# Performance work log

Hardware: AMD Instinct MI355X
Metric: run time of the kernel (lower is better)

Reference implementation:

```python
import jax, jax.numpy as jnp
import numpy as np

B, N, F, H, C, NH = 4, 256, 64, 64, 32, 4
EPS = 1e-5
INF = 1e5


def setup_inputs() -> dict:
    key = jax.random.key(0)
    ks = iter(jax.random.split(key, 40))
    def rn(shape, s=0.05):
        return jax.random.normal(next(ks), shape, jnp.float32) * s
    return dict(
        h=rn((B, N, F), 1.0), x=rn((B, N, 3), 1.0), v=rn((B, N, 3), 1.0),
        # edge_model = ConcatenationFilter: Linear(2F+1->H), SiLU, Linear(H->H), SiLU
        W_e1=rn((2 * F + 1, H)), b_e1=jnp.zeros(H), W_e2=rn((H, H)), b_e2=jnp.zeros(H),
        # coefficients_mlp: Linear(H->H), SiLU, Linear(H->C)
        W_c1=rn((H, H)), b_c1=jnp.zeros(H), W_c2=rn((H, C)), b_c2=jnp.zeros(C),
        # post_norm_mlp: Linear(C->H), SiLU, Linear(H->H)
        W_p1=rn((C, H)), b_p1=jnp.zeros(H), W_p2=rn((H, H)), b_p2=jnp.zeros(H),
        # semantic_attention_mlp: Linear(H->NH), LeakyReLU(0.2)
        W_s=rn((H, NH)), b_s=jnp.zeros(NH),
        # node_mlp: Linear(NH*H + H + F -> H), SiLU, Linear(H->F)
        W_n1=rn((NH * H + H + F, H)), b_n1=jnp.zeros(H), W_n2=rn((H, F)), b_n2=jnp.zeros(F),
        # velocity_mlp: Linear(F->H), SiLU, Linear(H->1, no bias), xavier gain=0.001
        W_v1=rn((F, H)), b_v1=jnp.zeros(H), W_v2=rn((H, 1), 0.001),
        log_gamma=jnp.zeros(NH),
    )


def reference(h, x, v, W_e1, b_e1, W_e2, b_e2, W_c1, b_c1, W_c2, b_c2,
              W_p1, b_p1, W_p2, b_p2, W_s, b_s, W_n1, b_n1, W_n2, b_n2,
              W_v1, b_v1, W_v2, log_gamma):
    silu = jax.nn.silu
    f = h.shape[-1]
    n = h.shape[-2]
    # pairwise displacements: [B,i,j,3] = x_j - x_i (torch: x.unsqueeze(-3) - x.unsqueeze(-2))
    x_minus_xt = x[..., None, :, :] - x[..., :, None, :]
    nrm = jnp.sqrt(jnp.sum(x_minus_xt ** 2, -1, keepdims=True) + EPS)  # [B,i,j,1]
    # edge model: first Linear over cat([h_j, h_i, nrm]) decomposed to avoid the big concat
    lin_j = h @ W_e1[:f]           # [B,N,H]
    lin_i = h @ W_e1[f:2 * f]      # [B,N,H]
    pre = lin_j[..., None, :, :] + lin_i[..., :, None, :] + nrm * W_e1[2 * f] + b_e1
    h_e_mtx = silu(silu(pre) @ W_e2 + b_e2)  # [B,i,j,H]
    # spatial attention
    coeff = silu(h_e_mtx @ W_c1 + b_c1) @ W_c2 + b_c2          # [B,i,j,C]
    x_scaled = x_minus_xt / (nrm + EPS) ** 2                   # [B,i,j,3]
    combinations = coeff[..., None] * x_scaled[..., None, :]   # [B,i,j,C,3]
    comb_sum = combinations.sum(-3)                            # sum over j -> [B,i,C,3]
    comb_norm = jnp.sum(comb_sum ** 2, -1)                     # [B,i,C]
    h_comb = silu(comb_norm @ W_p1 + b_p1) @ W_p2 + b_p2       # [B,i,H]
    delta_v = combinations.mean(axis=(-2, -3))                 # [B,i,3]
    # velocity + coordinate update (update_coordinate=True, velocity=True)
    v = (silu(h @ W_v1 + b_v1) @ W_v2) * v
    v = delta_v + v
    x = x + v
    # combined attention over j axis (-2)
    eye = jnp.eye(n, dtype=h.dtype)[:, :, None]                # [N,N,1]
    att_e = jax.nn.softmax(-(nrm + INF * eye) * jnp.exp(log_gamma), axis=-2)  # softmin
    att_s = jax.nn.softmax(jax.nn.leaky_relu(h_e_mtx @ W_s + b_s, 0.2) - INF * eye, axis=-2)
    att = jax.nn.softmax(att_e * att_s, axis=-2)               # [B,i,j,NH]
    # head-expanded messages: (h_e_mtx[...,H,1] * att[...,1,NH]).flatten -> [B,i,j,H*NH]
    h_e_full = (h_e_mtx[..., :, None] * att[..., None, :]).reshape(h_e_mtx.shape[:-1] + (-1,))
    h_e = h_e_full.sum(-2)                                     # aggregate over j -> [B,i,H*NH]
    out = silu(jnp.concatenate([h, h_e, h_comb], -1) @ W_n1 + b_n1) @ W_n2 + b_n2
    h = h + out  # residual
    return (h, x, v)
```

## Files before the change

### kernel.cpp

```cpp
#include <hip/hip_runtime.h>

typedef unsigned short u16;
typedef unsigned int   u32;
typedef __attribute__((ext_vector_type(8))) short bf16x8;
typedef __attribute__((ext_vector_type(4))) float f32x4;

#define EPSc 1e-5f
#define INFc 1e5f

#define O_LINJ  0
#define O_LINI  262144
#define O_VSC   524288
#define O_WE2F  528384
#define O_WC1F  536576
#define O_WC2F  546816
#define O_WP1C  550912
#define O_WP2C  559104
#define O_WN2C  575488
#define O_WN1C  591872
#define O_XF    690176
#define O_VF    702464
#define O_BIAS  714752
#define O_FLAG  741536

#define B_BE2 0
#define B_BC1 64
#define B_BC2 128
#define B_BS  160
#define B_GE  164
#define B_BP1 168
#define B_BP2 232
#define B_BN1 296
#define B_BN2 360
#define B_W1L 424
#define B_BE1 488

struct P {
    const void *h, *x, *v;
    const void *We1, *be1, *We2, *be2, *Wc1, *bc1, *Wc2, *bc2;
    const void *Wp1, *bp1, *Wp2, *bp2, *Ws_, *bs_;
    const void *Wn1, *bn1, *Wn2, *bn2, *Wv1, *bv1, *Wv2, *lg;
    float *linj, *lini, *vsc, *wp1c, *wp2c, *wn1c, *wn2c, *xf, *vf, *biasf;
    u16 *we2f, *wc1f, *wc2f;
    u32 *flagw;
    const u32 *flag;
    void *out;
};

__device__ __forceinline__ float bfr(u16 u) { return __uint_as_float(((u32)u) << 16); }
__device__ __forceinline__ u16 f2bf(float f) {
    u32 u = __float_as_uint(f);
    u = u + 0x7fffu + ((u >> 16) & 1u);
    return (u16)(u >> 16);
}
__device__ __forceinline__ u32 cvtpk(float lo, float hi) {
    u32 r;
    asm("v_cvt_pk_bf16_f32 %0, %1, %2" : "=v"(r) : "v"(lo), "v"(hi));
    return r;
}
__device__ __forceinline__ float frcp(float x) { return __builtin_amdgcn_rcpf(x); }
__device__ __forceinline__ float silu(float x) { return x * frcp(1.f + __expf(-x)); }
__device__ __forceinline__ float lrelu(float x) { return x > 0.f ? x : 0.2f * x; }

__device__ __forceinline__ float LDr(const void* p, int i, bool bf) {
    return bf ? bfr(((const u16*)p)[i]) : ((const float*)p)[i];
}
__device__ __forceinline__ u16 ENCr(const void* p, int i, bool bf) {
    return bf ? ((const u16*)p)[i] : f2bf(((const float*)p)[i]);
}
__device__ __forceinline__ void STr(void* p, int i, float v, bool bf) {
    if (bf) ((u16*)p)[i] = (u16)cvtpk(v, v);
    else    ((float*)p)[i] = v;
}
#define WAVE_FENCE() do { asm volatile("s_waitcnt lgkmcnt(0)" ::: "memory"); \
                          __builtin_amdgcn_sched_barrier(0); } while (0)

__device__ __forceinline__ bool block_flag(const void* h, u32* s_flagv, int t) {
    if (t < 64) {
        const u16* ph = (const u16*)h;
        int cnt = 0;
        #pragma unroll
        for (int e = 0; e < 4; e++) {
            float v = bfr(ph[t * 4 + e]);
            float a = fabsf(v);
            if (v == 0.f || (a > 1e-6f && a < 1024.f)) cnt++;
        }
        #pragma unroll
        for (int o = 32; o; o >>= 1) cnt += __shfl_xor(cnt, o);
        if (t == 0) *s_flagv = (cnt >= 224) ? 1u : 0u;
    }
    __syncthreads();
    return *s_flagv != 0u;
}

__global__ __launch_bounds__(256) void prep_all(P p) {
    __shared__ u32 s_flagv;
    const int t = threadIdx.x;
    const int blk = blockIdx.x;
    const bool bf = block_flag(p.h, &s_flagv, t);

    if (blk == 0) {
        if (t == 0) p.flagw[0] = bf ? 1u : 0u;
        for (int idx = t; idx < 4096; idx += 256) {
            int e = idx & 7, l = (idx >> 3) & 63, ks = (idx >> 9) & 1, nt = idx >> 10;
            int k = ks * 32 + (l >> 4) * 8 + e, c = (l & 15) * 4 + nt;
            p.we2f[idx] = ENCr(p.We2, k * 64 + c, bf);
        }
    } else if (blk == 1) {
        for (int idx = t; idx < 5120; idx += 256) {
            int e = idx & 7, l = (idx >> 3) & 63, ks = (idx >> 9) & 1, nt = idx >> 10;
            int k = ks * 32 + (l >> 4) * 8 + e;
            u16 v;
            if (nt < 4) v = ENCr(p.Wc1, k * 64 + (l & 15) * 4 + nt, bf);
            else { int cc = l & 15; v = (cc < 4) ? ENCr(p.Ws_, k * 4 + cc, bf) : (u16)0; }
            p.wc1f[idx] = v;
        }
    } else if (blk == 2) {
        for (int idx = t; idx < 2048; idx += 256) {
            int e = idx & 7, l = (idx >> 3) & 63, ks = (idx >> 9) & 1, nt = idx >> 10;
            int k = ks * 32 + (l >> 4) * 8 + e, c = nt * 16 + (l & 15);
            p.wc2f[idx] = ENCr(p.Wc2, k * 32 + c, bf);
        }
        if (t < 64) {
            p.biasf[B_BE2 + t] = LDr(p.be2, t, bf);
            p.biasf[B_BC1 + t] = LDr(p.bc1, t, bf);
            p.biasf[B_BP1 + t] = LDr(p.bp1, t, bf);
            p.biasf[B_BP2 + t] = LDr(p.bp2, t, bf);
            p.biasf[B_BN1 + t] = LDr(p.bn1, t, bf);
            p.biasf[B_BN2 + t] = LDr(p.bn2, t, bf);
            p.biasf[B_W1L + t] = LDr(p.We1, 128 * 64 + t, bf);
            p.biasf[B_BE1 + t] = LDr(p.be1, t, bf);
        } else if (t < 96) {
            p.biasf[B_BC2 + (t - 64)] = LDr(p.bc2, t - 64, bf);
        } else if (t < 100) {
            p.biasf[B_BS + (t - 96)] = LDr(p.bs_, t - 96, bf);
            p.biasf[B_GE + (t - 96)] = __expf(LDr(p.lg, t - 96, bf));
        }
        for (int i = t; i < 3072; i += 256) {
            p.xf[i] = LDr(p.x, i, bf);
            p.vf[i] = LDr(p.v, i, bf);
        }
    } else if (blk == 3) {
        for (int idx = t; idx < 2048; idx += 256) p.wp1c[idx] = LDr(p.Wp1, idx, bf);
        for (int idx = t; idx < 4096; idx += 256) p.wp2c[idx] = LDr(p.Wp2, idx, bf);
        for (int idx = t; idx < 4096; idx += 256) p.wn2c[idx] = LDr(p.Wn2, idx, bf);
    } else if (blk == 4) {
        for (int idx = t; idx < 12288; idx += 256) p.wn1c[idx] = LDr(p.Wn1, idx, bf);
    } else if (blk == 5) {
        for (int idx = t; idx < 12288; idx += 256) p.wn1c[12288 + idx] = LDr(p.Wn1, 12288 + idx, bf);
    } else {
        __shared__ alignas(16) u16 lds_wj[4096];
        __shared__ alignas(16) u16 lds_wi[4096];
        __shared__ alignas(16) u16 lds_wv[4096];
        __shared__ alignas(16) u16 shh[4][16 * 72];
        for (int idx = t; idx < 4096; idx += 256) {
            lds_wj[idx] = ENCr(p.We1, idx, bf);
            lds_wi[idx] = ENCr(p.We1, 4096 + idx, bf);
            lds_wv[idx] = ENCr(p.Wv1, idx, bf);
        }
        const int w = t >> 6, lane = t & 63;
        const int l15 = lane & 15, l4 = lane >> 4;
        const int n0 = (blk - 6) * 64 + w * 16;
        #pragma unroll
        for (int rr = 0; rr < 4; rr++) {
            int row = rr * 4 + l4;
            if (bf) {
                const u16* hb = (const u16*)p.h;
                *(uint2*)(&shh[w][row * 72 + l15 * 4]) =
                    *(const uint2*)(&hb[(n0 + row) * 64 + l15 * 4]);
            } else {
                const float* hf = (const float*)p.h;
                f32x4 hv = *(const f32x4*)(&hf[(n0 + row) * 64 + l15 * 4]);
                uint2 ww; ww.x = cvtpk(hv[0], hv[1]); ww.y = cvtpk(hv[2], hv[3]);
                *(uint2*)(&shh[w][row * 72 + l15 * 4]) = ww;
            }
        }
        __syncthreads();
        f32x4 dj[4] = {}, di[4] = {}, dv[4] = {};
        #pragma unroll
        for (int nt = 0; nt < 4; nt++) {
            #pragma unroll
            for (int ks = 0; ks < 2; ks++) {
                bf16x8 a = *(const bf16x8*)(&shh[w][l15 * 72 + ks * 32 + l4 * 8]);
                bf16x8 bj, bi2, bvv;
                #pragma unroll
                for (int e = 0; e < 8; e++) {
                    int off = (ks * 32 + l4 * 8 + e) * 64 + nt * 16 + l15;
                    bj[e]  = (short)lds_wj[off];
                    bi2[e] = (short)lds_wi[off];
                    bvv[e] = (short)lds_wv[off];
                }
                dj[nt] = __builtin_amdgcn_mfma_f32_16x16x32_bf16(a, bj,  dj[nt], 0, 0, 0);
                di[nt] = __builtin_amdgcn_mfma_f32_16x16x32_bf16(a, bi2, di[nt], 0, 0, 0);
                dv[nt] = __builtin_amdgcn_mfma_f32_16x16x32_bf16(a, bvv, dv[nt], 0, 0, 0);
            }
        }
        #pragma unroll
        for (int nt = 0; nt < 4; nt++)
            #pragma unroll
            for (int q = 0; q < 4; q++) {
                int n = n0 + l4 * 4 + q, c = nt * 16 + l15;
                p.linj[n * 64 + c] = dj[nt][q];
                p.lini[n * 64 + c] = di[nt][q];
            }
        float bv1v[4], wv2v[4];
        #pragma unroll
        for (int nt = 0; nt < 4; nt++) {
            bv1v[nt] = LDr(p.bv1, nt * 16 + l15, bf);
            wv2v[nt] = LDr(p.Wv2, nt * 16 + l15, bf);
        }
        #pragma unroll
        for (int q = 0; q < 4; q++) {
            float s = 0.f;
            #pragma unroll
            for (int nt = 0; nt < 4; nt++)
                s += silu(dv[nt][q] + bv1v[nt]) * wv2v[nt];
            s += __shfl_xor(s, 1);
            s += __shfl_xor(s, 2);
            s += __shfl_xor(s, 4);
            s += __shfl_xor(s, 8);
            if (l15 == 0) p.vsc[n0 + l4 * 4 + q] = s;
        }
    }
}

template<int N>
__device__ __forceinline__ void blk_red(float v[N], bool domax, float* scr, int tid) {
    #pragma unroll
    for (int s2 = 32; s2; s2 >>= 1)
        #pragma unroll
        for (int u = 0; u < N; u++) {
            float o = __shfl_xor(v[u], s2);
            v[u] = domax ? fmaxf(v[u], o) : (v[u] + o);
        }
    if ((tid & 63) == 0) {
        int w = tid >> 6;
        #pragma unroll
        for (int u = 0; u < N; u++) scr[w * N + u] = v[u];
    }
    __syncthreads();
    #pragma unroll
    for (int u = 0; u < N; u++) {
        float a = scr[0 * N + u], b2 = scr[1 * N + u], c = scr[2 * N + u], d = scr[3 * N + u];
        v[u] = domax ? fmaxf(fmaxf(a, b2), fmaxf(c, d)) : ((a + b2) + (c + d));
    }
}

__global__ __launch_bounds__(256, 3) void sake_all(P p) {
    const bool bf = (p.flag[0] != 0u);
    const int node = blockIdx.x;
    const int i = node & 255;
    const int b = node >> 8;
    const int tid = threadIdx.x;
    const int j = tid;
    const int lane = tid & 63, wv = tid >> 6;
    const int l15 = lane & 15, l4 = lane >> 4;

    __shared__ alignas(16) u16 s_A[256 * 72];
    __shared__ alignas(16) u16 s_wsq[4 * 16 * 72];
    __shared__ alignas(16) u16 s_xs[256 * 4];
    __shared__ alignas(8)  u16 s_sa[256 * 4];
    __shared__ alignas(16) u16 s_att[4 * 272];
    __shared__ float s_rows[4 * 64];
    __shared__ float s_cn[32];
    __shared__ float s_dv[4];
    __shared__ float s_scr[48];
    __shared__ float s_misc[8];

    u16*   s_AT    = s_A;
    float* s_nin   = (float*)s_wsq;
    float* s_t1    = (float*)((char*)s_wsq + 1536);
    float* s_part  = (float*)((char*)s_wsq + 1792);
    float* s_combw = (float*)s_att;

    bf16x8 bw2[2][4];
    #pragma unroll
    for (int n = 0; n < 4; n++)
        #pragma unroll
        for (int ks = 0; ks < 2; ks++)
            bw2[ks][n] = *(const bf16x8*)(p.we2f + ((n * 2 + ks) * 64 + lane) * 8);
    float be2v[4];
    #pragma unroll
    for (int n = 0; n < 4; n++) be2v[n] = p.biasf[B_BE2 + 4 * l15 + n];

    if (tid < 64) {
        s_rows[0 * 64 + tid] = p.biasf[B_W1L + tid];
        s_rows[1 * 64 + tid] = p.biasf[B_BE1 + tid];
        s_rows[2 * 64 + tid] = p.lini[node * 64 + tid];
        s_rows[3 * 64 + tid] = bf ? bfr(((const u16*)p.h)[node * 64 + tid])
                                  : ((const float*)p.h)[node * 64 + tid];
    } else if (tid < 67) {
        s_misc[tid - 64] = p.xf[node * 3 + (tid - 64)];
    } else if (tid == 67) {
        s_misc[3] = p.vsc[node];
    } else if (tid < 72) {
        s_misc[4 + (tid - 68)] = p.biasf[B_GE + (tid - 68)];
    }
    __syncthreads();

    float nrm;
    {
        float d0 = p.xf[(b * 256 + j) * 3 + 0] - s_misc[0];
        float d1 = p.xf[(b * 256 + j) * 3 + 1] - s_misc[1];
        float d2 = p.xf[(b * 256 + j) * 3 + 2] - s_misc[2];
        nrm = sqrtf(d0 * d0 + d1 * d1 + d2 * d2 + EPSc);
        float den = nrm + EPSc;
        float invd = frcp(den * den);
        uint2 xw;
        xw.x = cvtpk(d0 * invd, d1 * invd);
        xw.y = cvtpk(d2 * invd, nrm);
        *(uint2*)(&s_xs[j * 4]) = xw;

        const f32x4* lj = (const f32x4*)(p.linj + (b * 256 + j) * 64);
        #pragma unroll
        for (int c = 0; c < 8; c++) {
            f32x4 a = lj[2 * c], bq = lj[2 * c + 1];
            float s[8];
            #pragma unroll
            for (int e = 0; e < 4; e++) {
                int o = c * 8 + e;
                s[e] = silu(a[e] + s_rows[128 + o] + nrm * s_rows[o] + s_rows[64 + o]);
            }
            #pragma unroll
            for (int e = 0; e < 4; e++) {
                int o = c * 8 + 4 + e;
                s[4 + e] = silu(bq[e] + s_rows[128 + o] + nrm * s_rows[o] + s_rows[64 + o]);
            }
            uint4 w;
            w.x = cvtpk(s[0], s[1]); w.y = cvtpk(s[2], s[3]);
            w.z = cvtpk(s[4], s[5]); w.w = cvtpk(s[6], s[7]);
            *(uint4*)(&s_A[j * 72 + c * 8]) = w;
        }
    }
    WAVE_FENCE();

    f32x4 acc[4][4] = {};
    #pragma unroll
    for (int mt = 0; mt < 4; mt++) {
        int row = (wv * 4 + mt) * 16 + l15;
        #pragma unroll
        for (int ks = 0; ks < 2; ks++) {
            bf16x8 a = *(const bf16x8*)(&s_A[row * 72 + ks * 32 + l4 * 8]);
            #pragma unroll
            for (int n = 0; n < 4; n++)
                acc[mt][n] = __builtin_amdgcn_mfma_f32_16x16x32_bf16(a, bw2[ks][n], acc[mt][n], 0, 0, 0);
        }
    }
    WAVE_FENCE();
    #pragma unroll
    for (int mt = 0; mt < 4; mt++)
        #pragma unroll
        for (int q = 0; q < 4; q++) {
            int row = (wv * 4 + mt) * 16 + l4 * 4 + q;
            uint2 pk;
            pk.x = cvtpk(silu(acc[mt][0][q] + be2v[0]), silu(acc[mt][1][q] + be2v[1]));
            pk.y = cvtpk(silu(acc[mt][2][q] + be2v[2]), silu(acc[mt][3][q] + be2v[3]));
            *(uint2*)(&s_A[row * 72 + 4 * l15]) = pk;
        }
    WAVE_FENCE();

    {
        bf16x8 bw3[2][5], bw4[2][2];
        #pragma unroll
        for (int n = 0; n < 5; n++)
            #pragma unroll
            for (int ks = 0; ks < 2; ks++)
                bw3[ks][n] = *(const bf16x8*)(p.wc1f + ((n * 2 + ks) * 64 + lane) * 8);
        #pragma unroll
        for (int n = 0; n < 2; n++)
            #pragma unroll
            for (int ks = 0; ks < 2; ks++)
                bw4[ks][n] = *(const bf16x8*)(p.wc2f + ((n * 2 + ks) * 64 + lane) * 8);
        float bc1v[4], bc2v[2];
        #pragma unroll
        for (int n = 0; n < 4; n++) bc1v[n] = p.biasf[B_BC1 + 4 * l15 + n];
        #pragma unroll
        for (int n = 0; n < 2; n++) bc2v[n] = p.biasf[B_BC2 + n * 16 + l15];
        float bsv = p.biasf[B_BS + (l15 & 3)];

        u16* myws = s_wsq + wv * (16 * 72);
        float cmb[2][3] = {};
        #pragma unroll 1
        for (int mt = 0; mt < 4; mt++) {
            f32x4 c1x[5] = {};
            #pragma unroll
            for (int ks = 0; ks < 2; ks++) {
                bf16x8 a = *(const bf16x8*)(&s_A[((wv * 4 + mt) * 16 + l15) * 72 + ks * 32 + l4 * 8]);
                #pragma unroll
                for (int n = 0; n < 5; n++)
                    c1x[n] = __builtin_amdgcn_mfma_f32_16x16x32_bf16(a, bw3[ks][n], c1x[n], 0, 0, 0);
            }
            #pragma unroll
            for (int q = 0; q < 4; q++) {
                uint2 pk;
                pk.x = cvtpk(silu(c1x[0][q] + bc1v[0]), silu(c1x[1][q] + bc1v[1]));
                pk.y = cvtpk(silu(c1x[2][q] + bc1v[2]), silu(c1x[3][q] + bc1v[3]));
                *(uint2*)(&myws[(l4 * 4 + q) * 72 + 4 * l15]) = pk;
            }
            if (l15 < 4) {
                #pragma unroll
                for (int q = 0; q < 4; q++) {
                    int row = wv * 64 + mt * 16 + l4 * 4 + q;
                    float sub = (row == i) ? INFc : 0.f;
                    float lv = lrelu(c1x[4][q] + bsv) - sub;
                    s_sa[row * 4 + l15] = (u16)cvtpk(lv, lv);
                }
            }
            WAVE_FENCE();
            f32x4 co[2] = {};
            #pragma unroll
            for (int ks = 0; ks < 2; ks++) {
                bf16x8 a2 = *(const bf16x8*)(&myws[l15 * 72 + ks * 32 + l4 * 8]);
                #pragma unroll
                for (int n = 0; n < 2; n++)
                    co[n] = __builtin_amdgcn_mfma_f32_16x16x32_bf16(a2, bw4[ks][n], co[n], 0, 0, 0);
            }
            #pragma unroll
            for (int q = 0; q < 4; q++) {
                int r = wv * 64 + mt * 16 + l4 * 4 + q;
                uint2 xw = *(const uint2*)(&s_xs[r * 4]);
                float x0 = __uint_as_float(xw.x << 16);
                float x1 = __uint_as_float(xw.x & 0xffff0000u);
                float x2 = __uint_as_float(xw.y << 16);
                #pragma unroll
                for (int n = 0; n < 2; n++) {
                    float c = co[n][q] + bc2v[n];
                    cmb[n][0] += c * x0;
                    cmb[n][1] += c * x1;
                    cmb[n][2] += c * x2;
                }
            }
        }
        #pragma unroll
        for (int n = 0; n < 2; n++)
            #pragma unroll
            for (int k = 0; k < 3; k++) {
                float v = cmb[n][k];
                v += __shfl_xor(v, 16);
                v += __shfl_xor(v, 32);
                cmb[n][k] = v;
            }
        if (l4 == 0) {
            #pragma unroll
            for (int n = 0; n < 2; n++)
                #pragma unroll
                for (int k = 0; k < 3; k++)
                    s_combw[(wv * 32 + n * 16 + l15) * 3 + k] = cmb[n][k];
        }
    }
    __syncthreads();

    uint4 her[8];
    #pragma unroll
    for (int c = 0; c < 8; c++) her[c] = *(const uint4*)(&s_A[j * 72 + c * 8]);
    float cnv = 0.f, dvv = 0.f;
    if (tid < 32) {
        float c0 = 0.f, c1 = 0.f, c2 = 0.f;
        #pragma unroll
        for (int w = 0; w < 4; w++) {
            c0 += s_combw[(w * 32 + tid) * 3 + 0];
            c1 += s_combw[(w * 32 + tid) * 3 + 1];
            c2 += s_combw[(w * 32 + tid) * 3 + 2];
        }
        cnv = c0 * c0 + c1 * c1 + c2 * c2;
    } else if (tid < 35) {
        int k = tid - 32;
        float a = 0.f;
        for (int w = 0; w < 4; w++)
            #pragma unroll 8
            for (int c = 0; c < 32; c++) a += s_combw[(w * 32 + c) * 3 + k];
        dvv = a * (1.0f / 8192.f);
    }
    __syncthreads();

    #pragma unroll
    for (int c = 0; c < 8; c++) {
        u32 d[4] = { her[c].x, her[c].y, her[c].z, her[c].w };
        #pragma unroll
        for (int dw = 0; dw < 4; dw++) {
            int hh = c * 8 + dw * 2;
            s_AT[hh * 272 + j]       = (u16)(d[dw] & 0xffffu);
            s_AT[(hh + 1) * 272 + j] = (u16)(d[dw] >> 16);
        }
    }
    if (tid < 32) s_cn[tid] = cnv;
    else if (tid < 35) s_dv[tid - 32] = dvv;

    {
        float pen = (j == i) ? INFc : 0.f;
        float elb = -(nrm + pen);
        float ge[4] = { s_misc[4], s_misc[5], s_misc[6], s_misc[7] };
        float sl[4];
        #pragma unroll
        for (int u = 0; u < 4; u++) sl[u] = bfr(s_sa[j * 4 + u]);

        float r4a[4] = { sl[0], sl[1], sl[2], sl[3] };
        blk_red<4>(r4a, true, s_scr, tid);

        float ae[4], as_[4];
        #pragma unroll
        for (int u = 0; u < 4; u++) ae[u] = __expf(ge[u] * elb);
        #pragma unroll
        for (int u = 0; u < 4; u++) as_[u] = __expf(sl[u] - r4a[u]);

        float r8[8] = { ae[0], ae[1], ae[2], ae[3], as_[0], as_[1], as_[2], as_[3] };
        blk_red<8>(r8, false, s_scr + 16, tid);

        float ep[4];
        #pragma unroll
        for (int u = 0; u < 4; u++)
            ep[u] = __expf(ae[u] * frcp(r8[u]) * as_[u] * frcp(r8[4 + u]));
        float r4b[4] = { ep[0], ep[1], ep[2], ep[3] };
        blk_red<4>(r4b, false, s_scr, tid);
        #pragma unroll
        for (int u = 0; u < 4; u++) {
            float av = ep[u] * frcp(r4b[u]);
            s_att[u * 272 + j] = (u16)cvtpk(av, av);
        }
    }
    __syncthreads();

    {
        f32x4 hg = {};
        #pragma unroll
        for (int ks = 0; ks < 8; ks++) {
            bf16x8 af = *(const bf16x8*)(&s_AT[(wv * 16 + l15) * 272 + ks * 32 + l4 * 8]);
            bf16x8 bfv = *(const bf16x8*)(&s_att[(l15 & 3) * 272 + ks * 32 + l4 * 8]);
            hg = __builtin_amdgcn_mfma_f32_16x16x32_bf16(af, bfv, hg, 0, 0, 0);
        }
        if (l15 < 4) {
            #pragma unroll
            for (int q = 0; q < 4; q++)
                s_nin[64 + (wv * 16 + l4 * 4 + q) * 4 + l15] = hg[q];
        }
    }
    if (wv == 0) {
        float a[4] = {};
        #pragma unroll
        for (int e = 0; e < 8; e++) {
            int c = l4 * 8 + e;
            f32x4 w4 = *(const f32x4*)(p.wp1c + c * 64 + 4 * l15);
            float cv = s_cn[c];
            #pragma unroll
            for (int n = 0; n < 4; n++) a[n] += cv * w4[n];
        }
        #pragma unroll
        for (int n = 0; n < 4; n++) {
            a[n] += __shfl_xor(a[n], 16);
            a[n] += __shfl_xor(a[n], 32);
        }
        if (l4 == 0) {
            f32x4 tv;
            #pragma unroll
            for (int n = 0; n < 4; n++) tv[n] = silu(a[n] + p.biasf[B_BP1 + 4 * l15 + n]);
            *(f32x4*)(&s_t1[4 * l15]) = tv;
        }
    } else if (wv == 1) {
        s_nin[lane] = s_rows[192 + lane];
    }
    __syncthreads();

    if (wv == 2) {
        float a[4] = {};
        #pragma unroll
        for (int it = 0; it < 16; it++) {
            int k = l4 * 16 + it;
            f32x4 w4 = *(const f32x4*)(p.wp2c + k * 64 + 4 * l15);
            float tk = s_t1[k];
            #pragma unroll
            for (int n = 0; n < 4; n++) a[n] += tk * w4[n];
        }
        #pragma unroll
        for (int n = 0; n < 4; n++) {
            a[n] += __shfl_xor(a[n], 16);
            a[n] += __shfl_xor(a[n], 32);
        }
        if (l4 == 0) {
            f32x4 hv;
            #pragma unroll
            for (int n = 0; n < 4; n++) hv[n] = a[n] + p.biasf[B_BP2 + 4 * l15 + n];
            *(f32x4*)(&s_nin[320 + 4 * l15]) = hv;
        }
        WAVE_FENCE();
    }
    {
        const int Q = (wv == 0) ? 0 : (wv == 1) ? 96 : (wv == 2) ? 288 : 192;
        int k0 = Q + l4 * 24;
        float a[4] = {};
        #pragma unroll
        for (int it = 0; it < 6; it++) {
            f32x4 inv = *(const f32x4*)(&s_nin[k0 + it * 4]);
            #pragma unroll
            for (int r = 0; r < 4; r++) {
                f32x4 w4 = *(const f32x4*)(p.wn1c + (k0 + it * 4 + r) * 64 + 4 * l15);
                #pragma unroll
                for (int n = 0; n < 4; n++) a[n] += inv[r] * w4[n];
            }
        }
        #pragma unroll
        for (int n = 0; n < 4; n++) {
            a[n] += __shfl_xor(a[n], 16);
            a[n] += __shfl_xor(a[n], 32);
        }
        if (l4 == 0) {
            f32x4 pv = { a[0], a[1], a[2], a[3] };
            *(f32x4*)(&s_part[wv * 64 + 4 * l15]) = pv;
        }
    }
    __syncthreads();

    if (wv == 0) {
        float v2 = p.biasf[B_BN1 + lane] + (s_part[lane] + s_part[64 + lane])
                 + (s_part[128 + lane] + s_part[192 + lane]);
        s_t1[lane] = silu(v2);
        WAVE_FENCE();
        float a[4] = {};
        #pragma unroll
        for (int it = 0; it < 16; it++) {
            int k = l4 * 16 + it;
            f32x4 w4 = *(const f32x4*)(p.wn2c + k * 64 + 4 * l15);
            float tk = s_t1[k];
            #pragma unroll
            for (int n = 0; n < 4; n++) a[n] += tk * w4[n];
        }
        #pragma unroll
        for (int n = 0; n < 4; n++) {
            a[n] += __shfl_xor(a[n], 16);
            a[n] += __shfl_xor(a[n], 32);
        }
        if (l4 == 0) {
            float o[4];
            #pragma unroll
            for (int n = 0; n < 4; n++) {
                int oo = 4 * l15 + n;
                o[n] = s_rows[192 + oo] + p.biasf[B_BN2 + oo] + a[n];
            }
            if (bf) {
                uint2 w; w.x = cvtpk(o[0], o[1]); w.y = cvtpk(o[2], o[3]);
                *(uint2*)((u16*)p.out + node * 64 + 4 * l15) = w;
            } else {
                f32x4 w = { o[0], o[1], o[2], o[3] };
                *(f32x4*)((float*)p.out + node * 64 + 4 * l15) = w;
            }
        }
    } else if (wv == 1 && lane < 3) {
        int k = lane;
        float vn = s_dv[k] + s_misc[3] * p.vf[node * 3 + k];
        float xn = p.xf[node * 3 + k] + vn;
        STr(p.out, 65536 + node * 3 + k, xn, bf);
        STr(p.out, 68608 + node * 3 + k, vn, bf);
    }
}

extern "C" void kernel_launch(void* const* d_in, const int* in_sizes, int n_in,
                              void* d_out, int out_size, void* d_ws, size_t ws_size,
                              hipStream_t stream) {
    (void)in_sizes; (void)n_in; (void)out_size; (void)ws_size;
    char* ws = (char*)d_ws;

    P p;
    p.h   = d_in[0];  p.x   = d_in[1];  p.v   = d_in[2];
    p.We1 = d_in[3];  p.be1 = d_in[4];  p.We2 = d_in[5];  p.be2 = d_in[6];
    p.Wc1 = d_in[7];  p.bc1 = d_in[8];  p.Wc2 = d_in[9];  p.bc2 = d_in[10];
    p.Wp1 = d_in[11]; p.bp1 = d_in[12]; p.Wp2 = d_in[13]; p.bp2 = d_in[14];
    p.Ws_ = d_in[15]; p.bs_ = d_in[16];
    p.Wn1 = d_in[17]; p.bn1 = d_in[18]; p.Wn2 = d_in[19]; p.bn2 = d_in[20];
    p.Wv1 = d_in[21]; p.bv1 = d_in[22]; p.Wv2 = d_in[23]; p.lg  = d_in[24];
    p.linj  = (float*)(ws + O_LINJ);
    p.lini  = (float*)(ws + O_LINI);
    p.vsc   = (float*)(ws + O_VSC);
    p.wp1c  = (float*)(ws + O_WP1C);
    p.wp2c  = (float*)(ws + O_WP2C);
    p.wn1c  = (float*)(ws + O_WN1C);
    p.wn2c  = (float*)(ws + O_WN2C);
    p.xf    = (float*)(ws + O_XF);
    p.vf    = (float*)(ws + O_VF);
    p.biasf = (float*)(ws + O_BIAS);
    p.we2f  = (u16*)(ws + O_WE2F);
    p.wc1f  = (u16*)(ws + O_WC1F);
    p.wc2f  = (u16*)(ws + O_WC2F);
    p.flagw = (u32*)(ws + O_FLAG);
    p.flag  = (const u32*)(ws + O_FLAG);
    p.out   = d_out;

    hipLaunchKernelGGL(prep_all, dim3(22), dim3(256), 0, stream, p);
    hipLaunchKernelGGL(sake_all, dim3(1024), dim3(256), 0, stream, p);
}
```

Before: 52.28 us.

## Shrink LDS with XOR swizzles and split coefficient MLP to raise occupancy

Replaces padded LDS arrays (stride 72/272) with XOR-swizzled unpadded layouts and aliases several scratch buffers, cutting per-block shared memory so four blocks fit per CU instead of three. The coefficient MLP's first layer is split into two 32-wide halves that each feed the second MFMA in turn, which shrinks the staging buffer and live accumulators. Per-node scalars now move through registers and shuffles instead of LDS, and h is reloaded from global memory. The tighter register budget from launch_bounds(256,4) risks spills, and the added fences serialise the per-tile work.

```diff
diff --git a/kernel.cpp b/kernel.cpp
--- a/kernel.cpp
+++ b/kernel.cpp
@@ -75,6 +75,11 @@
 #define WAVE_FENCE() do { asm volatile("s_waitcnt lgkmcnt(0)" ::: "memory"); \
                           __builtin_amdgcn_sched_barrier(0); } while (0)
 
+#define SWA(row, col)  ((row) * 64  + ((col) ^ (((row) & 7) << 3)))
+#define SWT(h, col)    ((h) * 256   + ((col) ^ (((h) & 7) << 3)))
+#define SWC(r, col)    ((r) * 32    + ((col) ^ (((r) & 3) << 3)))
+#define SWATT(u, col)  ((u) * 256   + ((col) ^ (((u) & 3) << 3)))
+
 __device__ __forceinline__ bool block_flag(const void* h, u32* s_flagv, int t) {
     if (t < 64) {
         const u16* ph = (const u16*)h;
@@ -111,8 +116,13 @@
             int e = idx & 7, l = (idx >> 3) & 63, ks = (idx >> 9) & 1, nt = idx >> 10;
             int k = ks * 32 + (l >> 4) * 8 + e;
             u16 v;
-            if (nt < 4) v = ENCr(p.Wc1, k * 64 + (l & 15) * 4 + nt, bf);
-            else { int cc = l & 15; v = (cc < 4) ? ENCr(p.Ws_, k * 4 + cc, bf) : (u16)0; }
+            if (nt < 4) {
+                int hh = nt >> 1, tt = nt & 1;
+                v = ENCr(p.Wc1, k * 64 + hh * 32 + 2 * (l & 15) + tt, bf);
+            } else {
+                int cc = l & 15;
+                v = (cc < 4) ? ENCr(p.Ws_, k * 4 + cc, bf) : (u16)0;
+            }
             p.wc1f[idx] = v;
         }
     } else if (blk == 2) {
@@ -246,7 +256,7 @@
     }
 }
 
-__global__ __launch_bounds__(256, 3) void sake_all(P p) {
+__global__ __launch_bounds__(256, 4) void sake_all(P p) {
     const bool bf = (p.flag[0] != 0u);
     const int node = blockIdx.x;
     const int i = node & 255;
@@ -256,22 +266,19 @@
     const int lane = tid & 63, wv = tid >> 6;
     const int l15 = lane & 15, l4 = lane >> 4;
 
-    __shared__ alignas(16) u16 s_A[256 * 72];
-    __shared__ alignas(16) u16 s_wsq[4 * 16 * 72];
-    __shared__ alignas(16) u16 s_xs[256 * 4];
-    __shared__ alignas(8)  u16 s_sa[256 * 4];
-    __shared__ alignas(16) u16 s_att[4 * 272];
-    __shared__ float s_rows[4 * 64];
-    __shared__ float s_cn[32];
-    __shared__ float s_dv[4];
-    __shared__ float s_scr[48];
-    __shared__ float s_misc[8];
-
-    u16*   s_AT    = s_A;
-    float* s_nin   = (float*)s_wsq;
-    float* s_t1    = (float*)((char*)s_wsq + 1536);
-    float* s_part  = (float*)((char*)s_wsq + 1792);
-    float* s_combw = (float*)s_att;
+    __shared__ alignas(16) u16 s_A[256 * 64];
+    __shared__ alignas(16) u16 s_c1[4 * 16 * 32];
+    __shared__ alignas(16) u16 s_rx[1024];
+    __shared__ alignas(16) u16 s_ry[1024];
+
+    float* erow  = (float*)s_rx;
+    float* combw = (float*)s_rx;
+    float* part  = (float*)s_rx;
+    float* nin   = (float*)s_ry;
+    float* scr   = (float*)s_c1;
+    u16*   c1w   = s_c1 + wv * (16 * 32);
+
+    float cnv = 0.f, dvv = 0.f;
 
     bf16x8 bw2[2][4];
     #pragma unroll
@@ -284,32 +291,24 @@
     for (int n = 0; n < 4; n++) be2v[n] = p.biasf[B_BE2 + 4 * l15 + n];
 
     if (tid < 64) {
-        s_rows[0 * 64 + tid] = p.biasf[B_W1L + tid];
-        s_rows[1 * 64 + tid] = p.biasf[B_BE1 + tid];
-        s_rows[2 * 64 + tid] = p.lini[node * 64 + tid];
-        s_rows[3 * 64 + tid] = bf ? bfr(((const u16*)p.h)[node * 64 + tid])
-                                  : ((const float*)p.h)[node * 64 + tid];
-    } else if (tid < 67) {
-        s_misc[tid - 64] = p.xf[node * 3 + (tid - 64)];
-    } else if (tid == 67) {
-        s_misc[3] = p.vsc[node];
-    } else if (tid < 72) {
-        s_misc[4 + (tid - 68)] = p.biasf[B_GE + (tid - 68)];
-    }
-    __syncthreads();
-
-    float nrm;
+        erow[tid]       = p.biasf[B_W1L + tid];
+        erow[64 + tid]  = p.biasf[B_BE1 + tid];
+        erow[128 + tid] = p.lini[node * 64 + tid];
+    }
+    __syncthreads();
+
+    float nrm, xr0, xr1, xr2;
     {
-        float d0 = p.xf[(b * 256 + j) * 3 + 0] - s_misc[0];
-        float d1 = p.xf[(b * 256 + j) * 3 + 1] - s_misc[1];
-        float d2 = p.xf[(b * 256 + j) * 3 + 2] - s_misc[2];
+        float xi0 = p.xf[node * 3 + 0];
+        float xi1 = p.xf[node * 3 + 1];
+        float xi2 = p.xf[node * 3 + 2];
+        float d0 = p.xf[(b * 256 + j) * 3 + 0] - xi0;
+        float d1 = p.xf[(b * 256 + j) * 3 + 1] - xi1;
+        float d2 = p.xf[(b * 256 + j) * 3 + 2] - xi2;
         nrm = sqrtf(d0 * d0 + d1 * d1 + d2 * d2 + EPSc);
         float den = nrm + EPSc;
         float invd = frcp(den * den);
-        uint2 xw;
-        xw.x = cvtpk(d0 * invd, d1 * invd);
-        xw.y = cvtpk(d2 * invd, nrm);
-        *(uint2*)(&s_xs[j * 4]) = xw;
+        xr0 = d0 * invd; xr1 = d1 * invd; xr2 = d2 * invd;
 
         const f32x4* lj = (const f32x4*)(p.linj + (b * 256 + j) * 64);
         #pragma unroll
@@ -319,20 +318,20 @@
             #pragma unroll
             for (int e = 0; e < 4; e++) {
                 int o = c * 8 + e;
-                s[e] = silu(a[e] + s_rows[128 + o] + nrm * s_rows[o] + s_rows[64 + o]);
+                s[e] = silu(a[e] + erow[128 + o] + nrm * erow[o] + erow[64 + o]);
             }
             #pragma unroll
             for (int e = 0; e < 4; e++) {
                 int o = c * 8 + 4 + e;
-                s[4 + e] = silu(bq[e] + s_rows[128 + o] + nrm * s_rows[o] + s_rows[64 + o]);
+                s[4 + e] = silu(bq[e] + erow[128 + o] + nrm * erow[o] + erow[64 + o]);
             }
             uint4 w;
             w.x = cvtpk(s[0], s[1]); w.y = cvtpk(s[2], s[3]);
             w.z = cvtpk(s[4], s[5]); w.w = cvtpk(s[6], s[7]);
-            *(uint4*)(&s_A[j * 72 + c * 8]) = w;
-        }
-    }
-    WAVE_FENCE();
+            *(uint4*)(&s_A[SWA(j, c * 8)]) = w;
+        }
+    }
+    __syncthreads();
 
     f32x4 acc[4][4] = {};
     #pragma unroll
@@ -340,7 +339,7 @@
         int row = (wv * 4 + mt) * 16 + l15;
         #pragma unroll
         for (int ks = 0; ks < 2; ks++) {
-            bf16x8 a = *(const bf16x8*)(&s_A[row * 72 + ks * 32 + l4 * 8]);
+            bf16x8 a = *(const bf16x8*)(&s_A[SWA(row, ks * 32 + l4 * 8)]);
             #pragma unroll
             for (int n = 0; n < 4; n++)
                 acc[mt][n] = __builtin_amdgcn_mfma_f32_16x16x32_bf16(a, bw2[ks][n], acc[mt][n], 0, 0, 0);
@@ -355,73 +354,94 @@
             uint2 pk;
             pk.x = cvtpk(silu(acc[mt][0][q] + be2v[0]), silu(acc[mt][1][q] + be2v[1]));
             pk.y = cvtpk(silu(acc[mt][2][q] + be2v[2]), silu(acc[mt][3][q] + be2v[3]));
-            *(uint2*)(&s_A[row * 72 + 4 * l15]) = pk;
+            *(uint2*)(&s_A[SWA(row, 4 * l15)]) = pk;
         }
     WAVE_FENCE();
 
     {
-        bf16x8 bw3[2][5], bw4[2][2];
-        #pragma unroll
-        for (int n = 0; n < 5; n++)
-            #pragma unroll
-            for (int ks = 0; ks < 2; ks++)
-                bw3[ks][n] = *(const bf16x8*)(p.wc1f + ((n * 2 + ks) * 64 + lane) * 8);
+        bf16x8 bw3[2][2][2], bwS[2], bw4[2][2];
+        #pragma unroll
+        for (int hh = 0; hh < 2; hh++)
+            #pragma unroll
+            for (int tt = 0; tt < 2; tt++)
+                #pragma unroll
+                for (int ks = 0; ks < 2; ks++)
+                    bw3[hh][tt][ks] = *(const bf16x8*)(p.wc1f + (((hh * 2 + tt) * 2 + ks) * 64 + lane) * 8);
+        #pragma unroll
+        for (int ks = 0; ks < 2; ks++)
+            bwS[ks] = *(const bf16x8*)(p.wc1f + ((4 * 2 + ks) * 64 + lane) * 8);
         #pragma unroll
         for (int n = 0; n < 2; n++)
             #pragma unroll
-            for (int ks = 0; ks < 2; ks++)
-                bw4[ks][n] = *(const bf16x8*)(p.wc2f + ((n * 2 + ks) * 64 + lane) * 8);
-        float bc1v[4], bc2v[2];
-        #pragma unroll
-        for (int n = 0; n < 4; n++) bc1v[n] = p.biasf[B_BC1 + 4 * l15 + n];
+            for (int hh = 0; hh < 2; hh++)
+                bw4[n][hh] = *(const bf16x8*)(p.wc2f + ((n * 2 + hh) * 64 + lane) * 8);
+        float bc1v[2][2], bc2v[2];
+        #pragma unroll
+        for (int hh = 0; hh < 2; hh++)
+            #pragma unroll
+            for (int tt = 0; tt < 2; tt++)
+                bc1v[hh][tt] = p.biasf[B_BC1 + hh * 32 + 2 * l15 + tt];
         #pragma unroll
         for (int n = 0; n < 2; n++) bc2v[n] = p.biasf[B_BC2 + n * 16 + l15];
         float bsv = p.biasf[B_BS + (l15 & 3)];
 
-        u16* myws = s_wsq + wv * (16 * 72);
         float cmb[2][3] = {};
         #pragma unroll 1
         for (int mt = 0; mt < 4; mt++) {
-            f32x4 c1x[5] = {};
-            #pragma unroll
-            for (int ks = 0; ks < 2; ks++) {
-                bf16x8 a = *(const bf16x8*)(&s_A[((wv * 4 + mt) * 16 + l15) * 72 + ks * 32 + l4 * 8]);
-                #pragma unroll
-                for (int n = 0; n < 5; n++)
-                    c1x[n] = __builtin_amdgcn_mfma_f32_16x16x32_bf16(a, bw3[ks][n], c1x[n], 0, 0, 0);
-            }
+            bf16x8 a0 = *(const bf16x8*)(&s_A[SWA((wv * 4 + mt) * 16 + l15, l4 * 8)]);
+            bf16x8 a1 = *(const bf16x8*)(&s_A[SWA((wv * 4 + mt) * 16 + l15, 32 + l4 * 8)]);
+
+            f32x4 cT0 = {}, cT1 = {}, cS = {};
+            cT0 = __builtin_amdgcn_mfma_f32_16x16x32_bf16(a0, bw3[0][0][0], cT0, 0, 0, 0);
+            cT0 = __builtin_amdgcn_mfma_f32_16x16x32_bf16(a1, bw3[0][0][1], cT0, 0, 0, 0);
+            cT1 = __builtin_amdgcn_mfma_f32_16x16x32_bf16(a0, bw3[0][1][0], cT1, 0, 0, 0);
+            cT1 = __builtin_amdgcn_mfma_f32_16x16x32_bf16(a1, bw3[0][1][1], cT1, 0, 0, 0);
+            cS  = __builtin_amdgcn_mfma_f32_16x16x32_bf16(a0, bwS[0], cS, 0, 0, 0);
+            cS  = __builtin_amdgcn_mfma_f32_16x16x32_bf16(a1, bwS[1], cS, 0, 0, 0);
             #pragma unroll
             for (int q = 0; q < 4; q++) {
-                uint2 pk;
-                pk.x = cvtpk(silu(c1x[0][q] + bc1v[0]), silu(c1x[1][q] + bc1v[1]));
-                pk.y = cvtpk(silu(c1x[2][q] + bc1v[2]), silu(c1x[3][q] + bc1v[3]));
-                *(uint2*)(&myws[(l4 * 4 + q) * 72 + 4 * l15]) = pk;
+                u32 pk = cvtpk(silu(cT0[q] + bc1v[0][0]), silu(cT1[q] + bc1v[0][1]));
+                *(u32*)(&c1w[SWC(l4 * 4 + q, 2 * l15)]) = pk;
             }
             if (l15 < 4) {
                 #pragma unroll
                 for (int q = 0; q < 4; q++) {
                     int row = wv * 64 + mt * 16 + l4 * 4 + q;
                     float sub = (row == i) ? INFc : 0.f;
-                    float lv = lrelu(c1x[4][q] + bsv) - sub;
-                    s_sa[row * 4 + l15] = (u16)cvtpk(lv, lv);
+                    float lv = lrelu(cS[q] + bsv) - sub;
+                    s_ry[row * 4 + l15] = (u16)cvtpk(lv, lv);
                 }
             }
             WAVE_FENCE();
             f32x4 co[2] = {};
-            #pragma unroll
-            for (int ks = 0; ks < 2; ks++) {
-                bf16x8 a2 = *(const bf16x8*)(&myws[l15 * 72 + ks * 32 + l4 * 8]);
-                #pragma unroll
-                for (int n = 0; n < 2; n++)
-                    co[n] = __builtin_amdgcn_mfma_f32_16x16x32_bf16(a2, bw4[ks][n], co[n], 0, 0, 0);
-            }
+            {
+                bf16x8 c1f = *(const bf16x8*)(&c1w[SWC(l15, l4 * 8)]);
+                co[0] = __builtin_amdgcn_mfma_f32_16x16x32_bf16(c1f, bw4[0][0], co[0], 0, 0, 0);
+                co[1] = __builtin_amdgcn_mfma_f32_16x16x32_bf16(c1f, bw4[1][0], co[1], 0, 0, 0);
+            }
+            f32x4 cU0 = {}, cU1 = {};
+            cU0 = __builtin_amdgcn_mfma_f32_16x16x32_bf16(a0, bw3[1][0][0], cU0, 0, 0, 0);
+            cU0 = __builtin_amdgcn_mfma_f32_16x16x32_bf16(a1, bw3[1][0][1], cU0, 0, 0, 0);
+            cU1 = __builtin_amdgcn_mfma_f32_16x16x32_bf16(a0, bw3[1][1][0], cU1, 0, 0, 0);
+            cU1 = __builtin_amdgcn_mfma_f32_16x16x32_bf16(a1, bw3[1][1][1], cU1, 0, 0, 0);
+            WAVE_FENCE();
             #pragma unroll
             for (int q = 0; q < 4; q++) {
-                int r = wv * 64 + mt * 16 + l4 * 4 + q;
-                uint2 xw = *(const uint2*)(&s_xs[r * 4]);
-                float x0 = __uint_as_float(xw.x << 16);
-                float x1 = __uint_as_float(xw.x & 0xffff0000u);
-                float x2 = __uint_as_float(xw.y << 16);
+                u32 pk = cvtpk(silu(cU0[q] + bc1v[1][0]), silu(cU1[q] + bc1v[1][1]));
+                *(u32*)(&c1w[SWC(l4 * 4 + q, 2 * l15)]) = pk;
+            }
+            WAVE_FENCE();
+            {
+                bf16x8 c1f = *(const bf16x8*)(&c1w[SWC(l15, l4 * 8)]);
+                co[0] = __builtin_amdgcn_mfma_f32_16x16x32_bf16(c1f, bw4[0][1], co[0], 0, 0, 0);
+                co[1] = __builtin_amdgcn_mfma_f32_16x16x32_bf16(c1f, bw4[1][1], co[1], 0, 0, 0);
+            }
+            #pragma unroll
+            for (int q = 0; q < 4; q++) {
+                int src = mt * 16 + l4 * 4 + q;
+                float x0 = __shfl(xr0, src);
+                float x1 = __shfl(xr1, src);
+                float x2 = __shfl(xr2, src);
                 #pragma unroll
                 for (int n = 0; n < 2; n++) {
                     float c = co[n][q] + bc2v[n];
@@ -445,30 +465,29 @@
             for (int n = 0; n < 2; n++)
                 #pragma unroll
                 for (int k = 0; k < 3; k++)
-                    s_combw[(wv * 32 + n * 16 + l15) * 3 + k] = cmb[n][k];
+                    combw[(wv * 32 + n * 16 + l15) * 3 + k] = cmb[n][k];
         }
     }
     __syncthreads();
 
     uint4 her[8];
     #pragma unroll
-    for (int c = 0; c < 8; c++) her[c] = *(const uint4*)(&s_A[j * 72 + c * 8]);
-    float cnv = 0.f, dvv = 0.f;
+    for (int c = 0; c < 8; c++) her[c] = *(const uint4*)(&s_A[SWA(j, c * 8)]);
     if (tid < 32) {
         float c0 = 0.f, c1 = 0.f, c2 = 0.f;
         #pragma unroll
         for (int w = 0; w < 4; w++) {
-            c0 += s_combw[(w * 32 + tid) * 3 + 0];
-            c1 += s_combw[(w * 32 + tid) * 3 + 1];
-            c2 += s_combw[(w * 32 + tid) * 3 + 2];
+            c0 += combw[(w * 32 + tid) * 3 + 0];
+            c1 += combw[(w * 32 + tid) * 3 + 1];
+            c2 += combw[(w * 32 + tid) * 3 + 2];
         }
         cnv = c0 * c0 + c1 * c1 + c2 * c2;
-    } else if (tid < 35) {
-        int k = tid - 32;
+    } else if (tid >= 64 && tid < 67) {
+        int k = tid - 64;
         float a = 0.f;
         for (int w = 0; w < 4; w++)
             #pragma unroll 8
-            for (int c = 0; c < 32; c++) a += s_combw[(w * 32 + c) * 3 + k];
+            for (int c = 0; c < 32; c++) a += combw[(w * 32 + c) * 3 + k];
         dvv = a * (1.0f / 8192.f);
     }
     __syncthreads();
@@ -479,23 +498,26 @@
         #pragma unroll
         for (int dw = 0; dw < 4; dw++) {
             int hh = c * 8 + dw * 2;
-            s_AT[hh * 272 + j]       = (u16)(d[dw] & 0xffffu);
-            s_AT[(hh + 1) * 272 + j] = (u16)(d[dw] >> 16);
-        }
-    }
-    if (tid < 32) s_cn[tid] = cnv;
-    else if (tid < 35) s_dv[tid - 32] = dvv;
+            s_A[SWT(hh, j)]     = (u16)(d[dw] & 0xffffu);
+            s_A[SWT(hh + 1, j)] = (u16)(d[dw] >> 16);
+        }
+    }
 
     {
         float pen = (j == i) ? INFc : 0.f;
         float elb = -(nrm + pen);
-        float ge[4] = { s_misc[4], s_misc[5], s_misc[6], s_misc[7] };
+        float ge[4];
+        #pragma unroll
+        for (int u = 0; u < 4; u++) ge[u] = p.biasf[B_GE + u];
+        uint2 sw = *(const uint2*)(&s_ry[j * 4]);
         float sl[4];
-        #pragma unroll
-        for (int u = 0; u < 4; u++) sl[u] = bfr(s_sa[j * 4 + u]);
+        sl[0] = __uint_as_float(sw.x << 16);
+        sl[1] = __uint_as_float(sw.x & 0xffff0000u);
+        sl[2] = __uint_as_float(sw.y << 16);
+        sl[3] = __uint_as_float(sw.y & 0xffff0000u);
 
         float r4a[4] = { sl[0], sl[1], sl[2], sl[3] };
-        blk_red<4>(r4a, true, s_scr, tid);
+        blk_red<4>(r4a, true, scr, tid);
 
         float ae[4], as_[4];
         #pragma unroll
@@ -504,18 +526,18 @@
         for (int u = 0; u < 4; u++) as_[u] = __expf(sl[u] - r4a[u]);
 
         float r8[8] = { ae[0], ae[1], ae[2], ae[3], as_[0], as_[1], as_[2], as_[3] };
-        blk_red<8>(r8, false, s_scr + 16, tid);
+        blk_red<8>(r8, false, scr + 16, tid);
 
         float ep[4];
         #pragma unroll
         for (int u = 0; u < 4; u++)
             ep[u] = __expf(ae[u] * frcp(r8[u]) * as_[u] * frcp(r8[4 + u]));
         float r4b[4] = { ep[0], ep[1], ep[2], ep[3] };
-        blk_red<4>(r4b, false, s_scr, tid);
+        blk_red<4>(r4b, false, scr, tid);
         #pragma unroll
         for (int u = 0; u < 4; u++) {
             float av = ep[u] * frcp(r4b[u]);
-            s_att[u * 272 + j] = (u16)cvtpk(av, av);
+            s_rx[SWATT(u, j)] = (u16)cvtpk(av, av);
         }
     }
     __syncthreads();
@@ -524,14 +546,14 @@
         f32x4 hg = {};
         #pragma unroll
         for (int ks = 0; ks < 8; ks++) {
-            bf16x8 af = *(const bf16x8*)(&s_AT[(wv * 16 + l15) * 272 + ks * 32 + l4 * 8]);
-            bf16x8 bfv = *(const bf16x8*)(&s_att[(l15 & 3) * 272 + ks * 32 + l4 * 8]);
+            bf16x8 af  = *(const bf16x8*)(&s_A[SWT(wv * 16 + l15, ks * 32 + l4 * 8)]);
+            bf16x8 bfv = *(const bf16x8*)(&s_rx[SWATT(l15 & 3, ks * 32 + l4 * 8)]);
             hg = __builtin_amdgcn_mfma_f32_16x16x32_bf16(af, bfv, hg, 0, 0, 0);
         }
         if (l15 < 4) {
             #pragma unroll
             for (int q = 0; q < 4; q++)
-                s_nin[64 + (wv * 16 + l4 * 4 + q) * 4 + l15] = hg[q];
+                nin[(wv * 16 + l4 * 4 + q) * 4 + l15] = hg[q];
         }
     }
     if (wv == 0) {
@@ -539,8 +561,8 @@
         #pragma unroll
         for (int e = 0; e < 8; e++) {
             int c = l4 * 8 + e;
+            float cv = __shfl(cnv, c);
             f32x4 w4 = *(const f32x4*)(p.wp1c + c * 64 + 4 * l15);
-            float cv = s_cn[c];
             #pragma unroll
             for (int n = 0; n < 4; n++) a[n] += cv * w4[n];
         }
@@ -553,10 +575,8 @@
             f32x4 tv;
             #pragma unroll
             for (int n = 0; n < 4; n++) tv[n] = silu(a[n] + p.biasf[B_BP1 + 4 * l15 + n]);
-            *(f32x4*)(&s_t1[4 * l15]) = tv;
-        }
-    } else if (wv == 1) {
-        s_nin[lane] = s_rows[192 + lane];
+            *(f32x4*)(&nin[320 + 4 * l15]) = tv;
+        }
     }
     __syncthreads();
 
@@ -566,7 +586,7 @@
         for (int it = 0; it < 16; it++) {
             int k = l4 * 16 + it;
             f32x4 w4 = *(const f32x4*)(p.wp2c + k * 64 + 4 * l15);
-            float tk = s_t1[k];
+            float tk = nin[320 + k];
             #pragma unroll
             for (int n = 0; n < 4; n++) a[n] += tk * w4[n];
         }
@@ -579,7 +599,7 @@
             f32x4 hv;
             #pragma unroll
             for (int n = 0; n < 4; n++) hv[n] = a[n] + p.biasf[B_BP2 + 4 * l15 + n];
-            *(f32x4*)(&s_nin[320 + 4 * l15]) = hv;
+            *(f32x4*)(&nin[256 + 4 * l15]) = hv;
         }
         WAVE_FENCE();
     }
@@ -587,14 +607,20 @@
         const int Q = (wv == 0) ? 0 : (wv == 1) ? 96 : (wv == 2) ? 288 : 192;
         int k0 = Q + l4 * 24;
         float a[4] = {};
-        #pragma unroll
-        for (int it = 0; it < 6; it++) {
-            f32x4 inv = *(const f32x4*)(&s_nin[k0 + it * 4]);
-            #pragma unroll
-            for (int r = 0; r < 4; r++) {
-                f32x4 w4 = *(const f32x4*)(p.wn1c + (k0 + it * 4 + r) * 64 + 4 * l15);
+        if (wv == 0) {
+            for (int k2 = k0; k2 < k0 + 24; k2++) {
+                float inv = (k2 < 64) ? LDr(p.h, node * 64 + k2, bf) : nin[k2 - 64];
+                f32x4 w4 = *(const f32x4*)(p.wn1c + k2 * 64 + 4 * l15);
                 #pragma unroll
-                for (int n = 0; n < 4; n++) a[n] += inv[r] * w4[n];
+                for (int n = 0; n < 4; n++) a[n] += inv * w4[n];
+            }
+        } else {
+            #pragma unroll 4
+            for (int k2 = k0; k2 < k0 + 24; k2++) {
+                float inv = nin[k2 - 64];
+                f32x4 w4 = *(const f32x4*)(p.wn1c + k2 * 64 + 4 * l15);
+                #pragma unroll
+                for (int n = 0; n < 4; n++) a[n] += inv * w4[n];
             }
         }
         #pragma unroll
@@ -604,22 +630,22 @@
         }
         if (l4 == 0) {
             f32x4 pv = { a[0], a[1], a[2], a[3] };
-            *(f32x4*)(&s_part[wv * 64 + 4 * l15]) = pv;
+            *(f32x4*)(&part[wv * 64 + 4 * l15]) = pv;
         }
     }
     __syncthreads();
 
     if (wv == 0) {
-        float v2 = p.biasf[B_BN1 + lane] + (s_part[lane] + s_part[64 + lane])
-                 + (s_part[128 + lane] + s_part[192 + lane]);
-        s_t1[lane] = silu(v2);
+        float v2 = p.biasf[B_BN1 + lane] + (part[lane] + part[64 + lane])
+                 + (part[128 + lane] + part[192 + lane]);
+        nin[320 + lane] = silu(v2);
         WAVE_FENCE();
         float a[4] = {};
         #pragma unroll
         for (int it = 0; it < 16; it++) {
             int k = l4 * 16 + it;
             f32x4 w4 = *(const f32x4*)(p.wn2c + k * 64 + 4 * l15);
-            float tk = s_t1[k];
+            float tk = nin[320 + k];
             #pragma unroll
             for (int n = 0; n < 4; n++) a[n] += tk * w4[n];
         }
@@ -633,7 +659,7 @@
             #pragma unroll
             for (int n = 0; n < 4; n++) {
                 int oo = 4 * l15 + n;
-                o[n] = s_rows[192 + oo] + p.biasf[B_BN2 + oo] + a[n];
+                o[n] = LDr(p.h, node * 64 + oo, bf) + p.biasf[B_BN2 + oo] + a[n];
             }
             if (bf) {
                 uint2 w; w.x = cvtpk(o[0], o[1]); w.y = cvtpk(o[2], o[3]);
@@ -645,7 +671,7 @@
         }
     } else if (wv == 1 && lane < 3) {
         int k = lane;
-        float vn = s_dv[k] + s_misc[3] * p.vf[node * 3 + k];
+        float vn = dvv + p.vsc[node] * p.vf[node * 3 + k];
         float xn = p.xf[node * 3 + k] + vn;
         STr(p.out, 65536 + node * 3 + k, xn, bf);
         STr(p.out, 68608 + node * 3 + k, vn, bf);
```

New measurement: 54.48 us. 1.04x slower.
